# Optimization experiments

Hardware: AMD Instinct MI355X
Metric: run time of the kernel (lower is better)

## Reference

```python
import jax, jax.numpy as jnp
import numpy as np

HIDDEN = 1024
EXPAND = 2
D_REC = HIDDEN * EXPAND
INTER = 4096
B, T = 4, 4096


def _rmsnorm(x, w, eps=1e-6):
    var = jnp.mean(x * x, axis=-1, keepdims=True)
    return x * jax.lax.rsqrt(var + eps) * w


def setup_inputs() -> dict:
    key = jax.random.key(0)
    ks = jax.random.split(key, 11)
    s = lambda fan: 1.0 / np.sqrt(fan)
    return {
        "x": jax.random.normal(ks[0], (B, T, HIDDEN), dtype=jnp.float32),
        "ln1_w": jnp.ones((HIDDEN,), dtype=jnp.float32),
        "ln2_w": jnp.ones((HIDDEN,), dtype=jnp.float32),
        "w_in": jax.random.normal(ks[1], (D_REC, HIDDEN), dtype=jnp.float32) * s(HIDDEN),
        "w_gate": jax.random.normal(ks[2], (D_REC, HIDDEN), dtype=jnp.float32) * s(HIDDEN),
        "a_param": jax.random.normal(ks[3], (D_REC,), dtype=jnp.float32) * 0.1,
        "w_a": jax.random.normal(ks[4], (D_REC, D_REC), dtype=jnp.float32) * s(D_REC),
        "w_out": jax.random.normal(ks[5], (HIDDEN, D_REC), dtype=jnp.float32) * s(D_REC),
        "w_mlp_gate": jax.random.normal(ks[6], (INTER, HIDDEN), dtype=jnp.float32) * s(HIDDEN),
        "w_mlp_up": jax.random.normal(ks[7], (INTER, HIDDEN), dtype=jnp.float32) * s(HIDDEN),
        "w_mlp_down": jax.random.normal(ks[8], (HIDDEN, INTER), dtype=jnp.float32) * s(INTER),
    }


def _hawk_scan(x_in, a):
    # x_in, a: [B, T, D_REC]; h_t = a_t*h_{t-1} + sqrt(1-a_t^2+eps)*x_t
    xs = jnp.moveaxis(x_in, 1, 0)  # [T, B, D]
    As = jnp.moveaxis(a, 1, 0)

    def step(state, inp):
        a_t, x_t = inp
        new = a_t * state + jnp.sqrt(1.0 - a_t * a_t + 1e-8) * x_t
        return new, new

    init = jnp.zeros(x_in.shape[::2], dtype=x_in.dtype)  # [B, D]
    _, ys = jax.lax.scan(step, init, (As, xs))
    return jnp.moveaxis(ys, 0, 1)  # [B, T, D]


def reference(x, ln1_w, ln2_w, w_in, w_gate, a_param, w_a, w_out,
              w_mlp_gate, w_mlp_up, w_mlp_down):
    h = _rmsnorm(x, ln1_w)
    x_in = h @ w_in.T                     # [B,T,D_REC]
    gate = jax.nn.sigmoid(h @ w_gate.T)
    a = jax.nn.sigmoid(a_param + x_in @ w_a.T)
    y = gate * _hawk_scan(x_in, a)
    x = x + y @ w_out.T
    h2 = _rmsnorm(x, ln2_w)
    mlp = (jax.nn.silu(h2 @ w_mlp_gate.T) * (h2 @ w_mlp_up.T)) @ w_mlp_down.T
    return x + mlp
```

## Files before the change

kernel.cpp:

```cpp
#include <hip/hip_runtime.h>
#include <cstdint>
#include <cmath>


typedef unsigned short u16;
typedef _Float16 f16;
typedef __bf16 bf16x8 __attribute__((ext_vector_type(8)));
typedef float  f32x4  __attribute__((ext_vector_type(4)));

#define BM 128
#define BN 128
#define BK 64

#define HID   1024
#define DREC  2048
#define INTER 4096
#define BT    16384
#define TLEN  4096
#define NCHAN 8192
#define CHUNK 64
#define NCH   64
#define NPAIR 4096

__device__ __forceinline__ float b2f(u16 u) {
  union { unsigned int i; float f; } v; v.i = ((unsigned int)u) << 16; return v.f;
}
__device__ __forceinline__ u16 f2bf(float f) {
  unsigned int u = __builtin_bit_cast(unsigned int, f);
  u += 0x7FFFu + ((u >> 16) & 1u);
  return (u16)(u >> 16);
}
__device__ __forceinline__ float sigm(float x) { return 1.f / (1.f + expf(-x)); }

typedef __attribute__((address_space(1))) void as1_void;
typedef __attribute__((address_space(3))) void as3_void;
__device__ __forceinline__ void async16(const void* g, void* l) {
  __builtin_amdgcn_global_load_lds((as1_void*)g, (as3_void*)l, 16, 0, 0);
}

__device__ __forceinline__ void xcd_remap(int& bx, int& by) {
  const int gx = gridDim.x, gy = gridDim.y;
  const int nwg = gx * gy;
  const int lid = blockIdx.x + gx * blockIdx.y;
  const int rid = (lid & 7) * (nwg >> 3) + (lid >> 3);
  bx = rid / gy;
  by = rid - bx * gy;
}

__global__ void f2b_all(const float* s0, const float* s1, const float* s2,
                        const float* s3, const float* s4, const float* s5,
                        const float* s6,
                        u16* d0, u16* d1, u16* d2, u16* d3, u16* d4, u16* d5,
                        u16* d6) {
  int blk = blockIdx.x;
  const float* src; u16* dst; int rel;
  if      (blk < 2048)  { src = s0; dst = d0; rel = blk; }
  else if (blk < 4096)  { src = s1; dst = d1; rel = blk - 2048; }
  else if (blk < 8192)  { src = s2; dst = d2; rel = blk - 4096; }
  else if (blk < 10240) { src = s3; dst = d3; rel = blk - 8192; }
  else if (blk < 14336) { src = s4; dst = d4; rel = blk - 10240; }
  else if (blk < 18432) { src = s5; dst = d5; rel = blk - 14336; }
  else                  { src = s6; dst = d6; rel = blk - 18432; }
  int i = rel * 256 + threadIdx.x;
  float4 v = ((const float4*)src)[i];
  ushort4 o;
  o.x = f2bf(v.x); o.y = f2bf(v.y); o.z = f2bf(v.z); o.w = f2bf(v.w);
  ((ushort4*)dst)[i] = o;
}

__global__ void rmsnorm_kernel(const float* __restrict__ x, const float* __restrict__ w,
                               u16* __restrict__ out) {
  const int row = blockIdx.x;
  const int tid = threadIdx.x;
  float4 v = ((const float4*)(x + (size_t)row * HID))[tid];
  float ss = v.x * v.x + v.y * v.y + v.z * v.z + v.w * v.w;
#pragma unroll
  for (int o = 32; o > 0; o >>= 1) ss += __shfl_down(ss, o);
  __shared__ float red[4];
  const int lane = tid & 63, wv = tid >> 6;
  if (lane == 0) red[wv] = ss;
  __syncthreads();
  float tot = red[0] + red[1] + red[2] + red[3];
  float sc = rsqrtf(tot * (1.f / (float)HID) + 1e-6f);
  float4 wv4 = ((const float4*)w)[tid];
  ushort4 o;
  o.x = f2bf(v.x * sc * wv4.x); o.y = f2bf(v.y * sc * wv4.y);
  o.z = f2bf(v.z * sc * wv4.z); o.w = f2bf(v.w * sc * wv4.w);
  ((ushort4*)(out + (size_t)row * HID))[tid] = o;
}

enum { EPI_LOGIT = 0, EPI_ADDF = 1 };

template <int EPI>
__global__ __launch_bounds__(256, 4)
void gemm1(const u16* __restrict__ A, const u16* __restrict__ W,
           int K, int N, int ldA, int ldW,
           float* outf, f16* outz, const float* auxf) {
  __shared__ alignas(16) u16 sA[BM * BK];
  __shared__ alignas(16) u16 sB[BN * BK];

  const int tid  = threadIdx.x;
  const int lane = tid & 63;
  const int wv   = tid >> 6;
  const int wm   = wv & 1;
  const int wn   = wv >> 1;
  const int lm   = lane & 15;
  const int quad = lane >> 4;

  int bx, by;
  xcd_remap(bx, by);
  const int row0 = bx * BM;
  const int col0 = by * BN;

  f32x4 acc[4][4];
#pragma unroll
  for (int i = 0; i < 4; ++i)
#pragma unroll
    for (int j = 0; j < 4; ++j) acc[i][j] = (f32x4)0.f;

  for (int k0 = 0; k0 < K; k0 += BK) {
#pragma unroll
    for (int i = 0; i < 4; ++i) {
      int p = i * 256 + tid;
      int r = p >> 3;
      int sg = (p & 7) ^ (r & 7);
      async16(A + (size_t)(row0 + r) * ldA + (k0 + sg * 8), (char*)sA + p * 16);
    }
#pragma unroll
    for (int i = 0; i < 4; ++i) {
      int p = i * 256 + tid;
      int r = p >> 3;
      int sg = (p & 7) ^ (r & 7);
      async16(W + (size_t)(col0 + r) * ldW + (k0 + sg * 8), (char*)sB + p * 16);
    }
    __syncthreads();

#pragma unroll
    for (int h = 0; h < 2; ++h) {
      bf16x8 af[4], bf[4];
#pragma unroll
      for (int mi = 0; mi < 4; ++mi) {
        int r = wm * 64 + mi * 16 + lm;
        af[mi] = ((const bf16x8*)sA)[r * 8 + ((h * 4 + quad) ^ (r & 7))];
      }
#pragma unroll
      for (int ni = 0; ni < 4; ++ni) {
        int c = wn * 64 + ni * 16 + lm;
        bf[ni] = ((const bf16x8*)sB)[c * 8 + ((h * 4 + quad) ^ (c & 7))];
      }
#pragma unroll
      for (int mi = 0; mi < 4; ++mi)
#pragma unroll
        for (int ni = 0; ni < 4; ++ni)
          acc[mi][ni] = __builtin_amdgcn_mfma_f32_16x16x32_bf16(af[mi], bf[ni], acc[mi][ni], 0, 0, 0);
    }
    __syncthreads();
  }

#pragma unroll
  for (int mi = 0; mi < 4; ++mi) {
    const int rbase = row0 + wm * 64 + mi * 16 + quad * 4;
#pragma unroll
    for (int ni = 0; ni < 4; ++ni) {
      const int cg = col0 + wn * 64 + ni * 16 + lm;
      f32x4 v = acc[mi][ni];
#pragma unroll
      for (int rr = 0; rr < 4; ++rr) {
        size_t idx = (size_t)(rbase + rr) * N + cg;
        float t = v[rr];
        if constexpr (EPI == EPI_LOGIT) {
          outz[idx] = (f16)(t + auxf[cg]);
        } else {
          outf[idx] = t + auxf[idx];
        }
      }
    }
  }
}

enum { EPI2_XG = 0, EPI2_SM = 1 };

template <int EPI>
__global__ __launch_bounds__(256, 4)
void gemm2(const u16* __restrict__ A, const u16* __restrict__ W0,
           const u16* __restrict__ W1,
           int K, int N, int ldA, int ldW,
           u16* out0, u16* out1) {
  __shared__ alignas(16) u16 sA[BM * BK];
  __shared__ alignas(16) u16 sB0[64 * BK];
  __shared__ alignas(16) u16 sB1[64 * BK];

  const int tid  = threadIdx.x;
  const int lane = tid & 63;
  const int wv   = tid >> 6;
  const int wm   = wv & 1;
  const int wn   = wv >> 1;
  const int lm   = lane & 15;
  const int quad = lane >> 4;

  const int row0 = blockIdx.x * BM;
  const int col0 = blockIdx.y * 64;

  f32x4 acc0[4][2], acc1[4][2];
#pragma unroll
  for (int i = 0; i < 4; ++i)
#pragma unroll
    for (int j = 0; j < 2; ++j) { acc0[i][j] = (f32x4)0.f; acc1[i][j] = (f32x4)0.f; }

  for (int k0 = 0; k0 < K; k0 += BK) {
#pragma unroll
    for (int i = 0; i < 4; ++i) {
      int p = i * 256 + tid;
      int r = p >> 3;
      int sg = (p & 7) ^ (r & 7);
      async16(A + (size_t)(row0 + r) * ldA + (k0 + sg * 8), (char*)sA + p * 16);
    }
#pragma unroll
    for (int i = 0; i < 2; ++i) {
      int p = i * 256 + tid;
      int r = p >> 3;
      int sg = (p & 7) ^ (r & 7);
      size_t go = (size_t)(col0 + r) * ldW + (k0 + sg * 8);
      async16(W0 + go, (char*)sB0 + p * 16);
      async16(W1 + go, (char*)sB1 + p * 16);
    }
    __syncthreads();

#pragma unroll
    for (int h = 0; h < 2; ++h) {
      bf16x8 af[4], b0[2], b1[2];
#pragma unroll
      for (int mi = 0; mi < 4; ++mi) {
        int r = wm * 64 + mi * 16 + lm;
        af[mi] = ((const bf16x8*)sA)[r * 8 + ((h * 4 + quad) ^ (r & 7))];
      }
#pragma unroll
      for (int ni = 0; ni < 2; ++ni) {
        int c = wn * 32 + ni * 16 + lm;
        int o = c * 8 + ((h * 4 + quad) ^ (c & 7));
        b0[ni] = ((const bf16x8*)sB0)[o];
        b1[ni] = ((const bf16x8*)sB1)[o];
      }
#pragma unroll
      for (int mi = 0; mi < 4; ++mi)
#pragma unroll
        for (int ni = 0; ni < 2; ++ni) {
          acc0[mi][ni] = __builtin_amdgcn_mfma_f32_16x16x32_bf16(af[mi], b0[ni], acc0[mi][ni], 0, 0, 0);
          acc1[mi][ni] = __builtin_amdgcn_mfma_f32_16x16x32_bf16(af[mi], b1[ni], acc1[mi][ni], 0, 0, 0);
        }
    }
    __syncthreads();
  }

#pragma unroll
  for (int mi = 0; mi < 4; ++mi) {
    const int rbase = row0 + wm * 64 + mi * 16 + quad * 4;
#pragma unroll
    for (int ni = 0; ni < 2; ++ni) {
      const int cg = col0 + wn * 32 + ni * 16 + lm;
#pragma unroll
      for (int rr = 0; rr < 4; ++rr) {
        size_t idx = (size_t)(rbase + rr) * N + cg;
        float v0 = acc0[mi][ni][rr];
        float v1 = acc1[mi][ni][rr];
        if constexpr (EPI == EPI2_XG) {
          out0[idx] = f2bf(v0);
          out1[idx] = f2bf(sigm(v1));
        } else {
          out0[idx] = f2bf(v0 * sigm(v0) * v1);
        }
      }
    }
  }
}

__global__ void scan_phase1(const f16* __restrict__ z, const u16* __restrict__ xin,
                            float2* __restrict__ ch_h, float2* __restrict__ ch_p) {
  int gtid = blockIdx.x * 256 + threadIdx.x;
  int c = gtid >> 12;
  int pair = gtid & (NPAIR - 1);
  int b = pair >> 10;
  int d = (pair & 1023) * 2;
  size_t base = ((size_t)b * TLEN + (size_t)c * CHUNK) * DREC + d;
  float2 h = {0.f, 0.f}, P = {1.f, 1.f};
#pragma unroll 8
  for (int t = 0; t < CHUNK; ++t) {
    size_t i = base + (size_t)t * DREC;
    f16 z2[2]; *(uint32_t*)z2 = *(const uint32_t*)(z + i);
    u16 x2[2]; *(uint32_t*)x2 = *(const uint32_t*)(xin + i);
    float a0 = sigm((float)z2[0]), a1 = sigm((float)z2[1]);
    h.x = a0 * h.x + sqrtf(1.f - a0 * a0 + 1e-8f) * b2f(x2[0]);
    h.y = a1 * h.y + sqrtf(1.f - a1 * a1 + 1e-8f) * b2f(x2[1]);
    P.x *= a0; P.y *= a1;
  }
  ch_h[gtid] = h;
  ch_p[gtid] = P;
}

__global__ void scan_phase2(float2* __restrict__ ch_h, const float2* __restrict__ ch_p) {
  int pair = blockIdx.x * 256 + threadIdx.x;
  float2 H = {0.f, 0.f};
#pragma unroll
  for (int c = 0; c < NCH; ++c) {
    int i = c * NPAIR + pair;
    float2 he = ch_h[i];
    float2 P  = ch_p[i];
    ch_h[i] = H;
    H.x = he.x + P.x * H.x;
    H.y = he.y + P.y * H.y;
  }
}

__global__ void scan_phase3(const f16* __restrict__ z, const u16* __restrict__ xin,
                            u16* gate_y, const float2* __restrict__ ch_h) {
  int gtid = blockIdx.x * 256 + threadIdx.x;
  int c = gtid >> 12;
  int pair = gtid & (NPAIR - 1);
  int b = pair >> 10;
  int d = (pair & 1023) * 2;
  size_t base = ((size_t)b * TLEN + (size_t)c * CHUNK) * DREC + d;
  float2 h = ch_h[gtid];
#pragma unroll 8
  for (int t = 0; t < CHUNK; ++t) {
    size_t i = base + (size_t)t * DREC;
    f16 z2[2]; *(uint32_t*)z2 = *(const uint32_t*)(z + i);
    u16 x2[2]; *(uint32_t*)x2 = *(const uint32_t*)(xin + i);
    u16 g2[2]; *(uint32_t*)g2 = *(const uint32_t*)(gate_y + i);
    float a0 = sigm((float)z2[0]), a1 = sigm((float)z2[1]);
    h.x = a0 * h.x + sqrtf(1.f - a0 * a0 + 1e-8f) * b2f(x2[0]);
    h.y = a1 * h.y + sqrtf(1.f - a1 * a1 + 1e-8f) * b2f(x2[1]);
    u16 o2[2];
    o2[0] = f2bf(b2f(g2[0]) * h.x);
    o2[1] = f2bf(b2f(g2[1]) * h.y);
    *(uint32_t*)(gate_y + i) = *(uint32_t*)o2;
  }
}

extern "C" void kernel_launch(void* const* d_in, const int* in_sizes, int n_in,
                              void* d_out, int out_size, void* d_ws, size_t ws_size,
                              hipStream_t stream) {
  const float* x      = (const float*)d_in[0];
  const float* ln1    = (const float*)d_in[1];
  const float* ln2    = (const float*)d_in[2];
  const float* w_in   = (const float*)d_in[3];
  const float* w_gate = (const float*)d_in[4];
  const float* a_par  = (const float*)d_in[5];
  const float* w_a    = (const float*)d_in[6];
  const float* w_out  = (const float*)d_in[7];
  const float* w_mg   = (const float*)d_in[8];
  const float* w_mu   = (const float*)d_in[9];
  const float* w_md   = (const float*)d_in[10];
  float* out = (float*)d_out;
  char* ws = (char*)d_ws;

  const size_t MB = 1024ull * 1024ull;
  u16* wb_in  = (u16*)(ws + 0 * MB);
  u16* wb_gt  = (u16*)(ws + 4 * MB);
  u16* wb_a   = (u16*)(ws + 8 * MB);
  u16* wb_out = (u16*)(ws + 16 * MB);
  u16* wb_mg  = (u16*)(ws + 20 * MB);
  u16* wb_mu  = (u16*)(ws + 28 * MB);
  u16* wb_md  = (u16*)(ws + 36 * MB);
  u16* hbuf  = (u16*)(ws + 44 * MB);
  f16* zbuf  = (f16*)(ws + 44 * MB);
  u16* gateb = (u16*)(ws + 108 * MB);
  u16* mbuf  = (u16*)(ws + 108 * MB);
  float2* chh = (float2*)(ws + 0 * MB);
  float2* chp = (float2*)(ws + 2 * MB);
  u16* xinb = (u16*)d_out;

  f2b_all<<<22528, 256, 0, stream>>>(w_in, w_gate, w_a, w_out, w_mg, w_mu, w_md,
                                     wb_in, wb_gt, wb_a, wb_out, wb_mg, wb_mu, wb_md);

  rmsnorm_kernel<<<BT, 256, 0, stream>>>(x, ln1, hbuf);

  gemm2<EPI2_XG><<<dim3(BT / BM, DREC / 64), 256, 0, stream>>>(
      hbuf, wb_in, wb_gt, HID, DREC, HID, HID, xinb, gateb);

  gemm1<EPI_LOGIT><<<dim3(BT / BM, DREC / BN), 256, 0, stream>>>(
      xinb, wb_a, DREC, DREC, DREC, DREC, nullptr, zbuf, a_par);

  scan_phase1<<<NCH * NPAIR / 256, 256, 0, stream>>>(zbuf, xinb, chh, chp);
  scan_phase2<<<NPAIR / 256, 256, 0, stream>>>(chh, chp);
  scan_phase3<<<NCH * NPAIR / 256, 256, 0, stream>>>(zbuf, xinb, gateb, chh);

  gemm1<EPI_ADDF><<<dim3(BT / BM, HID / BN), 256, 0, stream>>>(
      gateb, wb_out, DREC, HID, DREC, DREC, out, nullptr, x);

  rmsnorm_kernel<<<BT, 256, 0, stream>>>(out, ln2, hbuf);

  for (int half = 0; half < 2; ++half) {
    const u16* wmg_h = wb_mg + (size_t)half * 2048 * HID;
    const u16* wmu_h = wb_mu + (size_t)half * 2048 * HID;
    const u16* wmd_h = wb_md + (size_t)half * 2048;
    gemm2<EPI2_SM><<<dim3(BT / BM, 2048 / 64), 256, 0, stream>>>(
        hbuf, wmg_h, wmu_h, HID, 2048, HID, HID, mbuf, nullptr);
    gemm1<EPI_ADDF><<<dim3(BT / BM, HID / BN), 256, 0, stream>>>(
        mbuf, wmd_h, 2048, HID, 2048, INTER, out, nullptr, out);
  }
}
```

Baseline: 1.122 ms.

## Replace dual-weight GEMM with 8-wave double-buffered pipelined 256x128 kernel

```diff
diff --git a/kernel.cpp b/kernel.cpp
--- a/kernel.cpp
+++ b/kernel.cpp
@@ -37,6 +37,12 @@
 __device__ __forceinline__ void async16(const void* g, void* l) {
   __builtin_amdgcn_global_load_lds((as1_void*)g, (as3_void*)l, 16, 0, 0);
 }
+
+#define BARSYNC() do { __builtin_amdgcn_s_barrier(); __builtin_amdgcn_sched_barrier(0); } while (0)
+#define LGKM0()   do { asm volatile("s_waitcnt lgkmcnt(0)" ::: "memory"); __builtin_amdgcn_sched_barrier(0); } while (0)
+#define LGKM8()   do { asm volatile("s_waitcnt lgkmcnt(8)" ::: "memory"); } while (0)
+#define VMC(N)    do { asm volatile("s_waitcnt vmcnt(" #N ")" ::: "memory"); __builtin_amdgcn_sched_barrier(0); } while (0)
+#define FENCE()   do { asm volatile("" ::: "memory"); __builtin_amdgcn_sched_barrier(0); } while (0)
 
 __device__ __forceinline__ void xcd_remap(int& bx, int& by) {
   const int gx = gridDim.x, gy = gridDim.y;
@@ -89,6 +95,55 @@
   ((ushort4*)(out + (size_t)row * HID))[tid] = o;
 }
 
+__device__ __forceinline__ void stageG(const u16* __restrict__ g, int ldg,
+                                       int rb, int k0, u16* lbase, int tid,
+                                       int nthr) {
+#pragma unroll
+  for (int i = 0; i < 2; ++i) {
+    int p = i * nthr + tid;
+    int r = p >> 3;
+    int sg = (p & 7) ^ (r & 7);
+    async16(g + (size_t)(rb + r) * ldg + (k0 + sg * 8), (char*)lbase + p * 16);
+  }
+}
+
+__device__ __forceinline__ void readA4(bf16x8 (&af)[4][2], const u16* base,
+                                       int rbase, int quad) {
+#pragma unroll
+  for (int i = 0; i < 4; ++i) {
+    int r = rbase + i * 16;
+#pragma unroll
+    for (int ks = 0; ks < 2; ++ks)
+      af[i][ks] = ((const bf16x8*)base)[r * 8 + ((ks * 4 + quad) ^ (r & 7))];
+  }
+}
+__device__ __forceinline__ void readB2(bf16x8 (&bf)[2][2], const u16* base,
+                                       int rbase, int quad) {
+#pragma unroll
+  for (int i = 0; i < 2; ++i) {
+    int r = rbase + i * 16;
+#pragma unroll
+    for (int ks = 0; ks < 2; ++ks)
+      bf[i][ks] = ((const bf16x8*)base)[r * 8 + ((ks * 4 + quad) ^ (r & 7))];
+  }
+}
+
+template <int MI0, int NI0, int NA>
+__device__ __forceinline__ void mfmaQ(f32x4 (&acc)[8][NA],
+                                      const bf16x8 (&af)[4][2],
+                                      const bf16x8 (&bf)[2][2]) {
+  __builtin_amdgcn_s_setprio(1);
+#pragma unroll
+  for (int mi = 0; mi < 4; ++mi)
+#pragma unroll
+    for (int ni = 0; ni < 2; ++ni)
+#pragma unroll
+      for (int ks = 0; ks < 2; ++ks)
+        acc[MI0 + mi][NI0 + ni] = __builtin_amdgcn_mfma_f32_16x16x32_bf16(
+            af[mi][ks], bf[ni][ks], acc[MI0 + mi][NI0 + ni], 0, 0, 0);
+  __builtin_amdgcn_s_setprio(0);
+}
+
 enum { EPI_LOGIT = 0, EPI_ADDF = 1 };
 
 template <int EPI>
@@ -181,86 +236,105 @@
 enum { EPI2_XG = 0, EPI2_SM = 1 };
 
 template <int EPI>
-__global__ __launch_bounds__(256, 4)
-void gemm2(const u16* __restrict__ A, const u16* __restrict__ W0,
-           const u16* __restrict__ W1,
-           int K, int N, int ldA, int ldW,
-           u16* out0, u16* out1) {
-  __shared__ alignas(16) u16 sA[BM * BK];
-  __shared__ alignas(16) u16 sB0[64 * BK];
-  __shared__ alignas(16) u16 sB1[64 * BK];
-
+__global__ __launch_bounds__(512, 2)
+void gemm2p8(const u16* __restrict__ A, const u16* __restrict__ W0,
+             const u16* __restrict__ W1,
+             int K, int N, int ldA, int ldW,
+             u16* out0, u16* out1) {
+  __shared__ u16 sA[2][16384];
+  __shared__ u16 sB[2][16384];
   const int tid  = threadIdx.x;
-  const int lane = tid & 63;
-  const int wv   = tid >> 6;
-  const int wm   = wv & 1;
-  const int wn   = wv >> 1;
-  const int lm   = lane & 15;
-  const int quad = lane >> 4;
-
-  const int row0 = blockIdx.x * BM;
-  const int col0 = blockIdx.y * 64;
-
-  f32x4 acc0[4][2], acc1[4][2];
-#pragma unroll
-  for (int i = 0; i < 4; ++i)
+  const int lane = tid & 63, wv = tid >> 6;
+  const int wm   = wv >> 2, wn = wv & 3;
+  const int lm   = lane & 15, quad = lane >> 4;
+  const int row0 = blockIdx.x * 256, col0 = blockIdx.y * 128;
+  const int NT   = K >> 6, NI = NT >> 1;
+
+  f32x4 acc0[8][2], acc1[8][2];
+#pragma unroll
+  for (int i = 0; i < 8; ++i)
 #pragma unroll
     for (int j = 0; j < 2; ++j) { acc0[i][j] = (f32x4)0.f; acc1[i][j] = (f32x4)0.f; }
 
-  for (int k0 = 0; k0 < K; k0 += BK) {
-#pragma unroll
-    for (int i = 0; i < 4; ++i) {
-      int p = i * 256 + tid;
-      int r = p >> 3;
-      int sg = (p & 7) ^ (r & 7);
-      async16(A + (size_t)(row0 + r) * ldA + (k0 + sg * 8), (char*)sA + p * 16);
-    }
-#pragma unroll
-    for (int i = 0; i < 2; ++i) {
-      int p = i * 256 + tid;
-      int r = p >> 3;
-      int sg = (p & 7) ^ (r & 7);
-      size_t go = (size_t)(col0 + r) * ldW + (k0 + sg * 8);
-      async16(W0 + go, (char*)sB0 + p * 16);
-      async16(W1 + go, (char*)sB1 + p * 16);
-    }
-    __syncthreads();
-
-#pragma unroll
-    for (int h = 0; h < 2; ++h) {
-      bf16x8 af[4], b0[2], b1[2];
-#pragma unroll
-      for (int mi = 0; mi < 4; ++mi) {
-        int r = wm * 64 + mi * 16 + lm;
-        af[mi] = ((const bf16x8*)sA)[r * 8 + ((h * 4 + quad) ^ (r & 7))];
-      }
-#pragma unroll
-      for (int ni = 0; ni < 2; ++ni) {
-        int c = wn * 32 + ni * 16 + lm;
-        int o = c * 8 + ((h * 4 + quad) ^ (c & 7));
-        b0[ni] = ((const bf16x8*)sB0)[o];
-        b1[ni] = ((const bf16x8*)sB1)[o];
-      }
-#pragma unroll
-      for (int mi = 0; mi < 4; ++mi)
-#pragma unroll
-        for (int ni = 0; ni < 2; ++ni) {
-          acc0[mi][ni] = __builtin_amdgcn_mfma_f32_16x16x32_bf16(af[mi], b0[ni], acc0[mi][ni], 0, 0, 0);
-          acc1[mi][ni] = __builtin_amdgcn_mfma_f32_16x16x32_bf16(af[mi], b1[ni], acc1[mi][ni], 0, 0, 0);
-        }
-    }
-    __syncthreads();
-  }
-
-#pragma unroll
-  for (int mi = 0; mi < 4; ++mi) {
-    const int rbase = row0 + wm * 64 + mi * 16 + quad * 4;
+  stageG(W0, ldW, col0,       0, sB[0],        tid, 512);
+  stageG(A,  ldA, row0,       0, sA[0],        tid, 512);
+  stageG(W1, ldW, col0,       0, sB[0] + 8192, tid, 512);
+  stageG(A,  ldA, row0 + 128, 0, sA[0] + 8192, tid, 512);
+  FENCE();
+  stageG(W0, ldW, col0, 64, sB[1], tid, 512);
+  stageG(A,  ldA, row0, 64, sA[1], tid, 512);
+  VMC(4);
+  BARSYNC();
+
+  for (int j = 0; j < NI; ++j) {
+    const int t  = j << 1;
+    const int k1 = (t + 1) * 64, k2 = (t + 2) * 64, k3 = (t + 3) * 64;
+    const bool s2 = (t + 2 < NT), s3 = (t + 3 < NT);
+    bf16x8 afL[4][2], afH[4][2], bf0[2][2], bf1[2][2];
+
+    readA4(afL, sA[0], wm * 128 + lm, quad);
+    readB2(bf0, sB[0], wn * 32 + lm, quad);
+    stageG(W1, ldW, col0, k1, sB[1] + 8192, tid, 512);
+    LGKM8();
+    BARSYNC(); LGKM0();
+    mfmaQ<0, 0>(acc0, afL, bf0);
+    BARSYNC();
+
+    readB2(bf1, sB[0] + 8192, wn * 32 + lm, quad);
+    stageG(A, ldA, row0 + 128, k1, sA[1] + 8192, tid, 512);
+    BARSYNC(); LGKM0();
+    mfmaQ<0, 0>(acc1, afL, bf1);
+    BARSYNC();
+
+    readA4(afH, sA[0], wm * 128 + 64 + lm, quad);
+    if (s2) stageG(W0, ldW, col0, k2, sB[0], tid, 512);
+    BARSYNC(); LGKM0();
+    mfmaQ<4, 0>(acc1, afH, bf1);
+    BARSYNC();
+
+    if (s2) { stageG(A, ldA, row0, k2, sA[0], tid, 512); VMC(4); }
+    else    { VMC(0); }
+    BARSYNC();
+    mfmaQ<4, 0>(acc0, afH, bf0);
+    BARSYNC();
+
+    readA4(afL, sA[1], wm * 128 + lm, quad);
+    readB2(bf0, sB[1], wn * 32 + lm, quad);
+    if (s2) stageG(W1, ldW, col0, k2, sB[0] + 8192, tid, 512);
+    LGKM8();
+    BARSYNC(); LGKM0();
+    mfmaQ<0, 0>(acc0, afL, bf0);
+    BARSYNC();
+
+    readB2(bf1, sB[1] + 8192, wn * 32 + lm, quad);
+    if (s2) stageG(A, ldA, row0 + 128, k2, sA[0] + 8192, tid, 512);
+    BARSYNC(); LGKM0();
+    mfmaQ<0, 0>(acc1, afL, bf1);
+    BARSYNC();
+
+    readA4(afH, sA[1], wm * 128 + 64 + lm, quad);
+    if (s3) stageG(W0, ldW, col0, k3, sB[1], tid, 512);
+    BARSYNC(); LGKM0();
+    mfmaQ<4, 0>(acc1, afH, bf1);
+    BARSYNC();
+
+    if (s3) { stageG(A, ldA, row0, k3, sA[1], tid, 512); VMC(4); }
+    else if (s2) { VMC(0); }
+    else { VMC(0); }
+    BARSYNC();
+    mfmaQ<4, 0>(acc0, afH, bf0);
+    BARSYNC();
+  }
+
+#pragma unroll
+  for (int mi = 0; mi < 8; ++mi) {
+    const int rb = row0 + wm * 128 + mi * 16 + quad * 4;
 #pragma unroll
     for (int ni = 0; ni < 2; ++ni) {
       const int cg = col0 + wn * 32 + ni * 16 + lm;
 #pragma unroll
       for (int rr = 0; rr < 4; ++rr) {
-        size_t idx = (size_t)(rbase + rr) * N + cg;
+        size_t idx = (size_t)(rb + rr) * N + cg;
         float v0 = acc0[mi][ni][rr];
         float v1 = acc1[mi][ni][rr];
         if constexpr (EPI == EPI2_XG) {
@@ -374,7 +448,7 @@
 
   rmsnorm_kernel<<<BT, 256, 0, stream>>>(x, ln1, hbuf);
 
-  gemm2<EPI2_XG><<<dim3(BT / BM, DREC / 64), 256, 0, stream>>>(
+  gemm2p8<EPI2_XG><<<dim3(BT / 256, DREC / 128), 512, 0, stream>>>(
       hbuf, wb_in, wb_gt, HID, DREC, HID, HID, xinb, gateb);
 
   gemm1<EPI_LOGIT><<<dim3(BT / BM, DREC / BN), 256, 0, stream>>>(
@@ -393,7 +467,7 @@
     const u16* wmg_h = wb_mg + (size_t)half * 2048 * HID;
     const u16* wmu_h = wb_mu + (size_t)half * 2048 * HID;
     const u16* wmd_h = wb_md + (size_t)half * 2048;
-    gemm2<EPI2_SM><<<dim3(BT / BM, 2048 / 64), 256, 0, stream>>>(
+    gemm2p8<EPI2_SM><<<dim3(BT / 256, 2048 / 128), 512, 0, stream>>>(
         hbuf, wmg_h, wmu_h, HID, 2048, HID, HID, mbuf, nullptr);
     gemm1<EPI_ADDF><<<dim3(BT / BM, HID / BN), 256, 0, stream>>>(
         mbuf, wmd_h, 2048, HID, 2048, INTER, out, nullptr, out);
```

Measured after the change: 1.214 ms. 8.2% more time.
